# Kernel optimization log

Measured on AMD Instinct MI355X. Metric: run time of the kernel, lower is better.

Reference implementation:

```python
import jax, jax.numpy as jnp
import numpy as np

N_NODES = 50000
N_EDGES = 1600000
D_IN = 128
D_OUT = 128
K_HOPS = 2


def setup_inputs() -> dict:
    key = jax.random.key(0)
    k1, k2, k3, k4 = jax.random.split(key, 4)
    feat = jax.random.normal(k1, (N_NODES, D_IN), dtype=jnp.float32)
    src = jax.random.randint(k2, (N_EDGES,), 0, N_NODES, dtype=jnp.int64)
    dst = jax.random.randint(k3, (N_EDGES,), 0, N_NODES, dtype=jnp.int64)
    # Linear params (xavier_uniform for W, zeros for b, as in reset_parameters)
    limit = float(np.sqrt(6.0 / (D_IN + D_OUT)))
    W = jax.random.uniform(k4, (D_OUT, D_IN), minval=-limit, maxval=limit, dtype=jnp.float32)
    b = jnp.zeros((D_OUT,), dtype=jnp.float32)
    return {"feat": feat, "src": src, "dst": dst, "W": W, "b": b}


def reference(feat, src, dst, W, b):
    # in-degrees: number of edges pointing into each node, clamped at 1
    ones = jnp.ones((src.shape[0],), dtype=jnp.float32)
    degs = jax.ops.segment_sum(ones, dst, num_segments=N_NODES)
    norm = jnp.clip(degs, 1.0, None) ** -0.5  # [N]
    norm = norm[:, None]  # [N,1]
    for _ in range(K_HOPS):
        feat = feat * norm                      # D^{-1/2} scale
        msg = feat[src]                         # copy_u: [E, D]
        feat = jax.ops.segment_sum(msg, dst, num_segments=N_NODES)  # sum into dst
        feat = feat * norm                      # D^{-1/2} scale
    # fc: Linear(in_feats, out_feats)
    return feat @ W.T + b
```

## Files before the change

### kernel.cpp

```cpp
#include <hip/hip_runtime.h>
#include <hip/hip_bf16.h>

#define NN 50000
#define NE 1600000
#define DD 128
#define NB 196
#define NCH 256
#define PER 6250
#define NT 8
#define TS 6250

typedef short bfrag __attribute__((ext_vector_type(8)));
typedef float ffrag __attribute__((ext_vector_type(4)));
typedef float f32x2 __attribute__((ext_vector_type(2)));

__device__ __forceinline__ float bf2f(unsigned short u) {
    union { unsigned int i; float f; } c; c.i = ((unsigned int)u) << 16; return c.f;
}
__device__ __forceinline__ unsigned short f2bf(float f) {
    __hip_bfloat16 h = __float2bfloat16(f);
    union { __hip_bfloat16 h; unsigned short u; } c; c.h = h; return c.u;
}
__device__ __forceinline__ int insane_bf16(unsigned short u) {
    unsigned e = (u >> 7) & 0xFF;
    return (e == 0xFF) || (e >= 0x8E);
}

__global__ void k_detect(const int* __restrict__ srcw, const int* __restrict__ dstw,
                         const unsigned short* __restrict__ feat16,
                         const unsigned short* __restrict__ w16,
                         int* __restrict__ flags) {
    __shared__ int s_idx, s_feat, s_w;
    int tid = threadIdx.x;
    if (tid == 0) { s_idx = 0; s_feat = 0; s_w = 0; }
    __syncthreads();
    if (tid < 64) {
        int v = srcw[2 * tid + 1] | dstw[2 * tid + 1];
        if (v) atomicOr(&s_idx, 1);
    }
    if (insane_bf16(feat16[2 * tid]) || insane_bf16(feat16[2 * tid + 512]))
        atomicOr(&s_feat, 1);
    if (insane_bf16(w16[2 * tid]) || insane_bf16(w16[2 * tid + 512]))
        atomicOr(&s_w, 1);
    __syncthreads();
    if (tid == 0) { flags[0] = (s_idx == 0) ? 1 : 0; flags[1] = s_feat; flags[2] = s_w; }
}

__device__ __forceinline__ int load_idx(const void* p, int e, int is64) {
    long long v = is64 ? ((const long long*)p)[e] : (long long)((const int*)p)[e];
    int i = (int)v;
    return (i < 0) ? 0 : (i >= NN ? NN - 1 : i);
}

__global__ __launch_bounds__(256) void k_count(const void* __restrict__ dst,
        int* __restrict__ cnt, const int* __restrict__ flags) {
    __shared__ int lc[NB];
    int c = blockIdx.x, tid = threadIdx.x;
    if (tid < NB) lc[tid] = 0;
    __syncthreads();
    int lo = c * PER, hi = lo + PER; if (hi > NE) hi = NE;
    int is64 = flags[0];
    for (int e = lo + tid; e < hi; e += 256)
        atomicAdd(&lc[load_idx(dst, e, is64) >> 8], 1);
    __syncthreads();
    if (tid < NB) cnt[tid * NCH + c] = lc[tid];
}

__global__ __launch_bounds__(256) void k_scan2(const int* __restrict__ cnt,
        int* __restrict__ loff, int* __restrict__ binsum) {
    __shared__ int buf[256];
    int b = blockIdx.x, tid = threadIdx.x;
    int v = cnt[b * NCH + tid];
    buf[tid] = v;
    __syncthreads();
    for (int off = 1; off < 256; off <<= 1) {
        int t = (tid >= off) ? buf[tid - off] : 0;
        __syncthreads();
        buf[tid] += t;
        __syncthreads();
    }
    loff[b * NCH + tid] = buf[tid] - v;
    if (tid == 255) binsum[b] = buf[255];
}

__global__ __launch_bounds__(256) void k_scanbin(const int* __restrict__ binsum,
        int* __restrict__ binoff, int* __restrict__ rowptr) {
    __shared__ int buf[256];
    int tid = threadIdx.x;
    int v = (tid < NB) ? binsum[tid] : 0;
    buf[tid] = v;
    __syncthreads();
    for (int off = 1; off < 256; off <<= 1) {
        int t = (tid >= off) ? buf[tid - off] : 0;
        __syncthreads();
        buf[tid] += t;
        __syncthreads();
    }
    if (tid < NB) binoff[tid] = buf[tid] - v;
    if (tid == NB - 1) binoff[NB] = buf[tid];
    if (tid == 0) rowptr[NN] = NE;
}

__global__ __launch_bounds__(256) void k_stage(const void* __restrict__ src,
        const void* __restrict__ dst, const int* __restrict__ binoff,
        const int* __restrict__ loff, unsigned* __restrict__ staged,
        const int* __restrict__ flags) {
    __shared__ int cur[NB];
    int c = blockIdx.x, tid = threadIdx.x;
    if (tid < NB) cur[tid] = binoff[tid] + loff[tid * NCH + c];
    __syncthreads();
    int lo = c * PER, hi = lo + PER; if (hi > NE) hi = NE;
    int is64 = flags[0];
    for (int e = lo + tid; e < hi; e += 256) {
        int d = load_idx(dst, e, is64);
        int s = load_idx(src, e, is64);
        int pos = atomicAdd(&cur[d >> 8], 1);
        staged[pos] = ((unsigned)(d & 255) << 16) | (unsigned)s;
    }
}

__global__ __launch_bounds__(512) void k_fill(const unsigned* __restrict__ staged,
        const int* __restrict__ binoff, int* __restrict__ rowptr,
        float* __restrict__ norm, int* __restrict__ srclist) {
    __shared__ int cnt4[256 * NT];
    __shared__ int ntot[256];
    int b = blockIdx.x, tid = threadIdx.x;
    int lo = binoff[b], hi = binoff[b + 1];
    for (int i = tid; i < 256 * NT; i += 512) cnt4[i] = 0;
    __syncthreads();
    for (int k = lo + tid; k < hi; k += 512) {
        unsigned u = staged[k];
        atomicAdd(&cnt4[(u >> 16) * NT + (int)(u & 0xffff) / TS], 1);
    }
    __syncthreads();
    if (tid < 256) {
        int s = 0;
        #pragma unroll
        for (int t = 0; t < NT; ++t) s += cnt4[tid * NT + t];
        ntot[tid] = s;
    }
    __syncthreads();
    for (int off = 1; off < 256; off <<= 1) {
        int t = 0;
        if (tid < 256 && tid >= off) t = ntot[tid - off];
        __syncthreads();
        if (tid < 256) ntot[tid] += t;
        __syncthreads();
    }
    if (tid < 256) {
        int deg = 0;
        #pragma unroll
        for (int t = 0; t < NT; ++t) deg += cnt4[tid * NT + t];
        int start = lo + ntot[tid] - deg;
        int n = b * 256 + tid;
        if (n < NN) {
            rowptr[n] = start;
            norm[n] = rsqrtf(fmaxf((float)deg, 1.0f));
        }
        int c = start;
        #pragma unroll
        for (int t = 0; t < NT; ++t) {
            int v = cnt4[tid * NT + t];
            cnt4[tid * NT + t] = c;
            c += v;
        }
    }
    __syncthreads();
    for (int k = lo + tid; k < hi; k += 512) {
        unsigned u = staged[k];
        int s = (int)(u & 0xffff);
        int pos = atomicAdd(&cnt4[(u >> 16) * NT + s / TS], 1);
        srclist[pos] = s << 7;
    }
}

__global__ void k_prescale(const void* __restrict__ feat,
                           const float* __restrict__ norm,
                           unsigned short* __restrict__ X,
                           const int* __restrict__ flags) {
    int i = blockIdx.x * 256 + threadIdx.x;
    if (i >= NN * DD / 4) return;
    float nm = norm[i >> 5];
    float4 v;
    if (flags[1]) {
        v = ((const float4*)feat)[i];
    } else {
        ushort4 f = ((const ushort4*)feat)[i];
        v.x = bf2f(f.x); v.y = bf2f(f.y); v.z = bf2f(f.z); v.w = bf2f(f.w);
    }
    ushort4 o;
    o.x = f2bf(v.x * nm); o.y = f2bf(v.y * nm);
    o.z = f2bf(v.z * nm); o.w = f2bf(v.w * nm);
    ((ushort4*)X)[i] = o;
}

__device__ __forceinline__ f32x2 bfpair(unsigned u) {
    union { unsigned i; float f; } lo, hi;
    lo.i = u << 16;
    hi.i = u & 0xffff0000u;
    f32x2 r; r[0] = lo.f; r[1] = hi.f; return r;
}
__device__ __forceinline__ void accp(f32x2* a, uint4 v) {
    a[0] += bfpair(v.x);
    a[1] += bfpair(v.y);
    a[2] += bfpair(v.z);
    a[3] += bfpair(v.w);
}

__global__ __launch_bounds__(256, 6) void k_gather(const unsigned short* __restrict__ Xin,
        const int* __restrict__ rowptr, const int* __restrict__ srclist,
        const float* __restrict__ norm, unsigned short* __restrict__ outp,
        int mode) {
    int wid = (blockIdx.x * 256 + threadIdx.x) >> 6;
    int lane = threadIdx.x & 63;
    if (wid >= NN) return;
    int beg = rowptr[wid], end = rowptr[wid + 1];
    int g = lane >> 4;
    int c8 = (lane & 15) << 3;
    const unsigned short* xb = Xin + c8;
    f32x2 a[4];
    #pragma unroll
    for (int k = 0; k < 4; ++k) a[k] = (f32x2){0.f, 0.f};

    int j = beg + g;
    for (; j + 28 < end; j += 32) {
        int s0 = srclist[j];
        int s1 = srclist[j + 4];
        int s2 = srclist[j + 8];
        int s3 = srclist[j + 12];
        int s4 = srclist[j + 16];
        int s5 = srclist[j + 20];
        int s6 = srclist[j + 24];
        int s7 = srclist[j + 28];
        uint4 r0 = *(const uint4*)(xb + s0);
        uint4 r1 = *(const uint4*)(xb + s1);
        uint4 r2 = *(const uint4*)(xb + s2);
        uint4 r3 = *(const uint4*)(xb + s3);
        uint4 r4 = *(const uint4*)(xb + s4);
        uint4 r5 = *(const uint4*)(xb + s5);
        uint4 r6 = *(const uint4*)(xb + s6);
        uint4 r7 = *(const uint4*)(xb + s7);
        accp(a, r0); accp(a, r1); accp(a, r2); accp(a, r3);
        accp(a, r4); accp(a, r5); accp(a, r6); accp(a, r7);
    }
    for (; j + 12 < end; j += 16) {
        int s0 = srclist[j];
        int s1 = srclist[j + 4];
        int s2 = srclist[j + 8];
        int s3 = srclist[j + 12];
        uint4 r0 = *(const uint4*)(xb + s0);
        uint4 r1 = *(const uint4*)(xb + s1);
        uint4 r2 = *(const uint4*)(xb + s2);
        uint4 r3 = *(const uint4*)(xb + s3);
        accp(a, r0); accp(a, r1); accp(a, r2); accp(a, r3);
    }
    for (; j < end; j += 4) {
        int s = srclist[j];
        uint4 v = *(const uint4*)(xb + s);
        accp(a, v);
    }
    #pragma unroll
    for (int k = 0; k < 4; ++k) {
        a[k][0] += __shfl_xor(a[k][0], 16);
        a[k][1] += __shfl_xor(a[k][1], 16);
        a[k][0] += __shfl_xor(a[k][0], 32);
        a[k][1] += __shfl_xor(a[k][1], 32);
    }

    if (g == 0) {
        float nm = norm[wid];
        float sc = (mode == 0) ? nm * nm : nm;
        uint4 o;
        o.x = ((unsigned)f2bf(a[0][1] * sc) << 16) | (unsigned)f2bf(a[0][0] * sc);
        o.y = ((unsigned)f2bf(a[1][1] * sc) << 16) | (unsigned)f2bf(a[1][0] * sc);
        o.z = ((unsigned)f2bf(a[2][1] * sc) << 16) | (unsigned)f2bf(a[2][0] * sc);
        o.w = ((unsigned)f2bf(a[3][1] * sc) << 16) | (unsigned)f2bf(a[3][0] * sc);
        *(uint4*)(outp + wid * DD + c8) = o;
    }
}

__global__ __launch_bounds__(256) void k_gemm2(const unsigned short* __restrict__ Yb,
        const void* __restrict__ Wp, const void* __restrict__ bp,
        void* __restrict__ outp, const int* __restrict__ flags) {
    __shared__ unsigned short Wl[DD * 136];
    int tid = threadIdx.x;
    int wf32 = flags[2], of32 = flags[1];

    for (int i = tid; i < 8192; i += 256) {
        int r = i >> 6, cc = i & 63;
        unsigned pk;
        if (wf32) {
            float2 w = ((const float2*)Wp)[i];
            pk = ((unsigned)f2bf(w.y) << 16) | (unsigned)f2bf(w.x);
        } else {
            pk = ((const unsigned*)Wp)[i];
        }
        *(unsigned*)&Wl[r * 136 + cc * 2] = pk;
    }
    __syncthreads();

    int wave = tid >> 6, lane = tid & 63;
    int nb = blockIdx.x * 64 + wave * 16;
    int m = lane & 15, quad = lane >> 4;
    int arow = nb + m; if (arow >= NN) arow = NN - 1;
    const unsigned short* arp = Yb + arow * DD + quad * 8;

    ffrag acc[8];
    #pragma unroll
    for (int t = 0; t < 8; ++t) acc[t] = (ffrag){0.f, 0.f, 0.f, 0.f};

    #pragma unroll
    for (int c = 0; c < 4; ++c) {
        bfrag af = *(const bfrag*)(arp + c * 32);
        #pragma unroll
        for (int t = 0; t < 8; ++t) {
            bfrag bf = *(const bfrag*)&Wl[(t * 16 + m) * 136 + c * 32 + quad * 8];
            acc[t] = __builtin_amdgcn_mfma_f32_16x16x32_bf16(af, bf, acc[t], 0, 0, 0);
        }
    }

    #pragma unroll
    for (int t = 0; t < 8; ++t) {
        int o = t * 16 + m;
        float bias = wf32 ? ((const float*)bp)[o] : bf2f(((const unsigned short*)bp)[o]);
        #pragma unroll
        for (int r = 0; r < 4; ++r) {
            int n = nb + quad * 4 + r;
            if (n < NN) {
                float v = acc[t][r] + bias;
                if (of32) ((float*)outp)[n * DD + o] = v;
                else      ((unsigned short*)outp)[n * DD + o] = f2bf(v);
            }
        }
    }
}

extern "C" void kernel_launch(void* const* d_in, const int* in_sizes, int n_in,
                              void* d_out, int out_size, void* d_ws, size_t ws_size,
                              hipStream_t stream) {
    const void* feat = d_in[0];
    const void* src  = d_in[1];
    const void* dst  = d_in[2];
    const void* W    = d_in[3];
    const void* b    = d_in[4];

    char* wsb = (char*)d_ws;
    int*   flags   = (int*)wsb;
    int*   rowptr  = (int*)(wsb + 64);
    float* norm    = (float*)(wsb + 200128);
    int*   cnt     = (int*)(wsb + 400128);
    int*   loff    = (int*)(wsb + 600832);
    int*   binsum  = (int*)(wsb + 801536);
    int*   binoff  = (int*)(wsb + 802560);
    int*   srclist = (int*)(wsb + 803584);
    unsigned short* X1 = (unsigned short*)(wsb + 7203584);
    unsigned short* X2 = (unsigned short*)(wsb + 20003584);
    unsigned* staged   = (unsigned*)(wsb + 20003584);

    k_detect<<<1, 256, 0, stream>>>((const int*)src, (const int*)dst,
                                    (const unsigned short*)feat,
                                    (const unsigned short*)W, flags);
    k_count<<<NCH, 256, 0, stream>>>(dst, cnt, flags);
    k_scan2<<<NB, 256, 0, stream>>>(cnt, loff, binsum);
    k_scanbin<<<1, 256, 0, stream>>>(binsum, binoff, rowptr);
    k_stage<<<NCH, 256, 0, stream>>>(src, dst, binoff, loff, staged, flags);
    k_fill<<<NB, 512, 0, stream>>>(staged, binoff, rowptr, norm, srclist);
    k_prescale<<<(NN * DD / 4 + 255) / 256, 256, 0, stream>>>(feat, norm, X1, flags);
    k_gather<<<(NN + 3) / 4, 256, 0, stream>>>(X1, rowptr, srclist, norm, X2, 0);
    k_gather<<<(NN + 3) / 4, 256, 0, stream>>>(X2, rowptr, srclist, norm, X1, 1);
    k_gemm2<<<(NN + 63) / 64, 256, 0, stream>>>(X1, W, b, d_out, flags);
}
```

Before: 274.2 us.

## Load edge indices cooperatively per wave and shuffle them, padding with a zero row

The gather kernel now has each lane load one source index per batch of up to 64 edges and hands them out with wave shuffles. Each group then issues eight feature loads at once, and out-of-range slots point at a zero-filled pad row, so the three tail loops with dependent index loads go away. The prescale kernel writes zero pad rows after both feature buffers, the X2 and staged offsets move to make room, and the fill kernel's source binning goes from 8 to 4 tiles. The launch-bounds occupancy hint is also dropped. In exchange, nodes with few edges waste loads on the zero row, and register pressure may change.

```diff
diff --git a/kernel.cpp b/kernel.cpp
--- a/kernel.cpp
+++ b/kernel.cpp
@@ -7,8 +7,9 @@
 #define NB 196
 #define NCH 256
 #define PER 6250
-#define NT 8
-#define TS 6250
+#define NT 4
+#define TS 12500
+#define ZOFF (NN * DD)
 
 typedef short bfrag __attribute__((ext_vector_type(8)));
 typedef float ffrag __attribute__((ext_vector_type(4)));
@@ -177,9 +178,17 @@
 __global__ void k_prescale(const void* __restrict__ feat,
                            const float* __restrict__ norm,
                            unsigned short* __restrict__ X,
+                           unsigned short* __restrict__ X2,
                            const int* __restrict__ flags) {
     int i = blockIdx.x * 256 + threadIdx.x;
-    if (i >= NN * DD / 4) return;
+    const int total = NN * DD / 4;
+    if (i >= total) {
+        int r = i - total;
+        ushort4 z; z.x = 0; z.y = 0; z.z = 0; z.w = 0;
+        if (r < 32)      ((ushort4*)X)[total + r] = z;
+        else if (r < 64) ((ushort4*)X2)[total + (r - 32)] = z;
+        return;
+    }
     float nm = norm[i >> 5];
     float4 v;
     if (flags[1]) {
@@ -207,7 +216,7 @@
     a[3] += bfpair(v.w);
 }
 
-__global__ __launch_bounds__(256, 6) void k_gather(const unsigned short* __restrict__ Xin,
+__global__ __launch_bounds__(256) void k_gather(const unsigned short* __restrict__ Xin,
         const int* __restrict__ rowptr, const int* __restrict__ srclist,
         const float* __restrict__ norm, unsigned short* __restrict__ outp,
         int mode) {
@@ -222,42 +231,37 @@
     #pragma unroll
     for (int k = 0; k < 4; ++k) a[k] = (f32x2){0.f, 0.f};
 
-    int j = beg + g;
-    for (; j + 28 < end; j += 32) {
-        int s0 = srclist[j];
-        int s1 = srclist[j + 4];
-        int s2 = srclist[j + 8];
-        int s3 = srclist[j + 12];
-        int s4 = srclist[j + 16];
-        int s5 = srclist[j + 20];
-        int s6 = srclist[j + 24];
-        int s7 = srclist[j + 28];
-        uint4 r0 = *(const uint4*)(xb + s0);
-        uint4 r1 = *(const uint4*)(xb + s1);
-        uint4 r2 = *(const uint4*)(xb + s2);
-        uint4 r3 = *(const uint4*)(xb + s3);
-        uint4 r4 = *(const uint4*)(xb + s4);
-        uint4 r5 = *(const uint4*)(xb + s5);
-        uint4 r6 = *(const uint4*)(xb + s6);
-        uint4 r7 = *(const uint4*)(xb + s7);
-        accp(a, r0); accp(a, r1); accp(a, r2); accp(a, r3);
-        accp(a, r4); accp(a, r5); accp(a, r6); accp(a, r7);
-    }
-    for (; j + 12 < end; j += 16) {
-        int s0 = srclist[j];
-        int s1 = srclist[j + 4];
-        int s2 = srclist[j + 8];
-        int s3 = srclist[j + 12];
-        uint4 r0 = *(const uint4*)(xb + s0);
-        uint4 r1 = *(const uint4*)(xb + s1);
-        uint4 r2 = *(const uint4*)(xb + s2);
-        uint4 r3 = *(const uint4*)(xb + s3);
-        accp(a, r0); accp(a, r1); accp(a, r2); accp(a, r3);
-    }
-    for (; j < end; j += 4) {
-        int s = srclist[j];
-        uint4 v = *(const uint4*)(xb + s);
-        accp(a, v);
+    int j = beg;
+    while (j < end) {
+        int n = end - j;
+        if (n > 64) n = 64;
+        int li = (lane < n) ? lane : (n - 1);
+        int sv = srclist[j + li];
+        {
+            uint4 r[8];
+            #pragma unroll
+            for (int i = 0; i < 8; ++i) {
+                int k = g + 4 * i;
+                int s = __shfl(sv, k);
+                s = (k < n) ? s : ZOFF;
+                r[i] = *(const uint4*)(xb + s);
+            }
+            #pragma unroll
+            for (int i = 0; i < 8; ++i) accp(a, r[i]);
+        }
+        if (n > 32) {
+            uint4 r[8];
+            #pragma unroll
+            for (int i = 0; i < 8; ++i) {
+                int k = 32 + g + 4 * i;
+                int s = __shfl(sv, k);
+                s = (k < n) ? s : ZOFF;
+                r[i] = *(const uint4*)(xb + s);
+            }
+            #pragma unroll
+            for (int i = 0; i < 8; ++i) accp(a, r[i]);
+        }
+        j += n;
     }
     #pragma unroll
     for (int k = 0; k < 4; ++k) {
@@ -354,8 +358,8 @@
     int*   binoff  = (int*)(wsb + 802560);
     int*   srclist = (int*)(wsb + 803584);
     unsigned short* X1 = (unsigned short*)(wsb + 7203584);
-    unsigned short* X2 = (unsigned short*)(wsb + 20003584);
-    unsigned* staged   = (unsigned*)(wsb + 20003584);
+    unsigned short* X2 = (unsigned short*)(wsb + 20003840);
+    unsigned* staged   = (unsigned*)(wsb + 20003840);
 
     k_detect<<<1, 256, 0, stream>>>((const int*)src, (const int*)dst,
                                     (const unsigned short*)feat,
@@ -365,7 +369,7 @@
     k_scanbin<<<1, 256, 0, stream>>>(binsum, binoff, rowptr);
     k_stage<<<NCH, 256, 0, stream>>>(src, dst, binoff, loff, staged, flags);
     k_fill<<<NB, 512, 0, stream>>>(staged, binoff, rowptr, norm, srclist);
-    k_prescale<<<(NN * DD / 4 + 255) / 256, 256, 0, stream>>>(feat, norm, X1, flags);
+    k_prescale<<<NN * DD / 4 / 256 + 1, 256, 0, stream>>>(feat, norm, X1, X2, flags);
     k_gather<<<(NN + 3) / 4, 256, 0, stream>>>(X1, rowptr, srclist, norm, X2, 0);
     k_gather<<<(NN + 3) / 4, 256, 0, stream>>>(X2, rowptr, srclist, norm, X1, 1);
     k_gemm2<<<(NN + 63) / 64, 256, 0, stream>>>(X1, W, b, d_out, flags);
```

New measurement: 259.5 us. 5.4% less time.

## Gather two nodes per 16-lane group, interleaved across source-range tiles

Applied to the files above, without the earlier changes.

The gather kernel now gives each 16-lane group two whole destination nodes instead of splitting one node's edges across four groups. It walks both nodes' edges tile by tile, using per-node source-range boundaries (4 tiles of 12500 source rows) that the fill kernel now records, so all wavefronts touch a similar region of X at the same time. This drops the cross-group shuffle reduction and is meant to improve L2 locality. In exchange it adds per-lane load imbalance from varying degrees, a shorter unroll, an extra int4 table per node, and it removes the occupancy hint from the launch bounds.

```diff
diff --git a/kernel.cpp b/kernel.cpp
--- a/kernel.cpp
+++ b/kernel.cpp
@@ -7,8 +7,10 @@
 #define NB 196
 #define NCH 256
 #define PER 6250
-#define NT 8
-#define TS 6250
+#define NT 4
+#define TS 12500
+#define GWAVE 6252
+#define GBLK 1563
 
 typedef short bfrag __attribute__((ext_vector_type(8)));
 typedef float ffrag __attribute__((ext_vector_type(4)));
@@ -121,6 +123,7 @@
 
 __global__ __launch_bounds__(512) void k_fill(const unsigned* __restrict__ staged,
         const int* __restrict__ binoff, int* __restrict__ rowptr,
+        int4* __restrict__ tptr,
         float* __restrict__ norm, int* __restrict__ srclist) {
     __shared__ int cnt4[256 * NT];
     __shared__ int ntot[256];
@@ -133,12 +136,9 @@
         atomicAdd(&cnt4[(u >> 16) * NT + (int)(u & 0xffff) / TS], 1);
     }
     __syncthreads();
-    if (tid < 256) {
-        int s = 0;
-        #pragma unroll
-        for (int t = 0; t < NT; ++t) s += cnt4[tid * NT + t];
-        ntot[tid] = s;
-    }
+    if (tid < 256)
+        ntot[tid] = cnt4[tid * NT] + cnt4[tid * NT + 1]
+                  + cnt4[tid * NT + 2] + cnt4[tid * NT + 3];
     __syncthreads();
     for (int off = 1; off < 256; off <<= 1) {
         int t = 0;
@@ -148,22 +148,25 @@
         __syncthreads();
     }
     if (tid < 256) {
-        int deg = 0;
-        #pragma unroll
-        for (int t = 0; t < NT; ++t) deg += cnt4[tid * NT + t];
+        int v0 = cnt4[tid * NT], v1 = cnt4[tid * NT + 1];
+        int v2 = cnt4[tid * NT + 2], v3 = cnt4[tid * NT + 3];
+        int deg = v0 + v1 + v2 + v3;
         int start = lo + ntot[tid] - deg;
         int n = b * 256 + tid;
+        int4 tp;
+        tp.x = start;
+        tp.y = start + v0;
+        tp.z = start + v0 + v1;
+        tp.w = start + v0 + v1 + v2;
         if (n < NN) {
             rowptr[n] = start;
             norm[n] = rsqrtf(fmaxf((float)deg, 1.0f));
-        }
-        int c = start;
-        #pragma unroll
-        for (int t = 0; t < NT; ++t) {
-            int v = cnt4[tid * NT + t];
-            cnt4[tid * NT + t] = c;
-            c += v;
-        }
+            tptr[n] = tp;
+        }
+        cnt4[tid * NT + 0] = tp.x;
+        cnt4[tid * NT + 1] = tp.y;
+        cnt4[tid * NT + 2] = tp.z;
+        cnt4[tid * NT + 3] = tp.w;
     }
     __syncthreads();
     for (int k = lo + tid; k < hi; k += 512) {
@@ -207,75 +210,90 @@
     a[3] += bfpair(v.w);
 }
 
-__global__ __launch_bounds__(256, 6) void k_gather(const unsigned short* __restrict__ Xin,
-        const int* __restrict__ rowptr, const int* __restrict__ srclist,
+__global__ __launch_bounds__(256) void k_gather(const unsigned short* __restrict__ Xin,
+        const int* __restrict__ rowptr, const int4* __restrict__ tptr,
+        const int* __restrict__ srclist,
         const float* __restrict__ norm, unsigned short* __restrict__ outp,
         int mode) {
     int wid = (blockIdx.x * 256 + threadIdx.x) >> 6;
     int lane = threadIdx.x & 63;
-    if (wid >= NN) return;
-    int beg = rowptr[wid], end = rowptr[wid + 1];
-    int g = lane >> 4;
+    int grp = lane >> 4;
     int c8 = (lane & 15) << 3;
     const unsigned short* xb = Xin + c8;
-    f32x2 a[4];
-    #pragma unroll
-    for (int k = 0; k < 4; ++k) a[k] = (f32x2){0.f, 0.f};
-
-    int j = beg + g;
-    for (; j + 28 < end; j += 32) {
-        int s0 = srclist[j];
-        int s1 = srclist[j + 4];
-        int s2 = srclist[j + 8];
-        int s3 = srclist[j + 12];
-        int s4 = srclist[j + 16];
-        int s5 = srclist[j + 20];
-        int s6 = srclist[j + 24];
-        int s7 = srclist[j + 28];
-        uint4 r0 = *(const uint4*)(xb + s0);
-        uint4 r1 = *(const uint4*)(xb + s1);
-        uint4 r2 = *(const uint4*)(xb + s2);
-        uint4 r3 = *(const uint4*)(xb + s3);
-        uint4 r4 = *(const uint4*)(xb + s4);
-        uint4 r5 = *(const uint4*)(xb + s5);
-        uint4 r6 = *(const uint4*)(xb + s6);
-        uint4 r7 = *(const uint4*)(xb + s7);
-        accp(a, r0); accp(a, r1); accp(a, r2); accp(a, r3);
-        accp(a, r4); accp(a, r5); accp(a, r6); accp(a, r7);
-    }
-    for (; j + 12 < end; j += 16) {
-        int s0 = srclist[j];
-        int s1 = srclist[j + 4];
-        int s2 = srclist[j + 8];
-        int s3 = srclist[j + 12];
-        uint4 r0 = *(const uint4*)(xb + s0);
-        uint4 r1 = *(const uint4*)(xb + s1);
-        uint4 r2 = *(const uint4*)(xb + s2);
-        uint4 r3 = *(const uint4*)(xb + s3);
-        accp(a, r0); accp(a, r1); accp(a, r2); accp(a, r3);
-    }
-    for (; j < end; j += 4) {
-        int s = srclist[j];
-        uint4 v = *(const uint4*)(xb + s);
-        accp(a, v);
-    }
-    #pragma unroll
-    for (int k = 0; k < 4; ++k) {
-        a[k][0] += __shfl_xor(a[k][0], 16);
-        a[k][1] += __shfl_xor(a[k][1], 16);
-        a[k][0] += __shfl_xor(a[k][0], 32);
-        a[k][1] += __shfl_xor(a[k][1], 32);
-    }
-
-    if (g == 0) {
-        float nm = norm[wid];
+
+    int n0 = wid * 8 + grp;
+    int n1 = n0 + 4;
+    bool val0 = (n0 < NN), val1 = (n1 < NN);
+
+    int4 tp0 = val0 ? tptr[n0] : (int4){0, 0, 0, 0};
+    int  e0  = val0 ? rowptr[n0 + 1] : 0;
+    int4 tp1 = val1 ? tptr[n1] : (int4){0, 0, 0, 0};
+    int  e1  = val1 ? rowptr[n1 + 1] : 0;
+
+    int st0[5] = {tp0.x, tp0.y, tp0.z, tp0.w, e0};
+    int st1[5] = {tp1.x, tp1.y, tp1.z, tp1.w, e1};
+
+    f32x2 a0[4], a1[4];
+    #pragma unroll
+    for (int k = 0; k < 4; ++k) { a0[k] = (f32x2){0.f, 0.f}; a1[k] = (f32x2){0.f, 0.f}; }
+
+    #pragma unroll
+    for (int t = 0; t < 4; ++t) {
+        int j = st0[t], je = st0[t + 1];
+        for (; j + 3 < je; j += 4) {
+            int s0 = srclist[j];
+            int s1 = srclist[j + 1];
+            int s2 = srclist[j + 2];
+            int s3 = srclist[j + 3];
+            uint4 r0 = *(const uint4*)(xb + s0);
+            uint4 r1 = *(const uint4*)(xb + s1);
+            uint4 r2 = *(const uint4*)(xb + s2);
+            uint4 r3 = *(const uint4*)(xb + s3);
+            accp(a0, r0); accp(a0, r1); accp(a0, r2); accp(a0, r3);
+        }
+        for (; j < je; ++j) {
+            int s = srclist[j];
+            uint4 v = *(const uint4*)(xb + s);
+            accp(a0, v);
+        }
+        j = st1[t]; je = st1[t + 1];
+        for (; j + 3 < je; j += 4) {
+            int s0 = srclist[j];
+            int s1 = srclist[j + 1];
+            int s2 = srclist[j + 2];
+            int s3 = srclist[j + 3];
+            uint4 r0 = *(const uint4*)(xb + s0);
+            uint4 r1 = *(const uint4*)(xb + s1);
+            uint4 r2 = *(const uint4*)(xb + s2);
+            uint4 r3 = *(const uint4*)(xb + s3);
+            accp(a1, r0); accp(a1, r1); accp(a1, r2); accp(a1, r3);
+        }
+        for (; j < je; ++j) {
+            int s = srclist[j];
+            uint4 v = *(const uint4*)(xb + s);
+            accp(a1, v);
+        }
+    }
+
+    if (val0) {
+        float nm = norm[n0];
         float sc = (mode == 0) ? nm * nm : nm;
         uint4 o;
-        o.x = ((unsigned)f2bf(a[0][1] * sc) << 16) | (unsigned)f2bf(a[0][0] * sc);
-        o.y = ((unsigned)f2bf(a[1][1] * sc) << 16) | (unsigned)f2bf(a[1][0] * sc);
-        o.z = ((unsigned)f2bf(a[2][1] * sc) << 16) | (unsigned)f2bf(a[2][0] * sc);
-        o.w = ((unsigned)f2bf(a[3][1] * sc) << 16) | (unsigned)f2bf(a[3][0] * sc);
-        *(uint4*)(outp + wid * DD + c8) = o;
+        o.x = ((unsigned)f2bf(a0[0][1] * sc) << 16) | (unsigned)f2bf(a0[0][0] * sc);
+        o.y = ((unsigned)f2bf(a0[1][1] * sc) << 16) | (unsigned)f2bf(a0[1][0] * sc);
+        o.z = ((unsigned)f2bf(a0[2][1] * sc) << 16) | (unsigned)f2bf(a0[2][0] * sc);
+        o.w = ((unsigned)f2bf(a0[3][1] * sc) << 16) | (unsigned)f2bf(a0[3][0] * sc);
+        *(uint4*)(outp + n0 * DD + c8) = o;
+    }
+    if (val1) {
+        float nm = norm[n1];
+        float sc = (mode == 0) ? nm * nm : nm;
+        uint4 o;
+        o.x = ((unsigned)f2bf(a1[0][1] * sc) << 16) | (unsigned)f2bf(a1[0][0] * sc);
+        o.y = ((unsigned)f2bf(a1[1][1] * sc) << 16) | (unsigned)f2bf(a1[1][0] * sc);
+        o.z = ((unsigned)f2bf(a1[2][1] * sc) << 16) | (unsigned)f2bf(a1[2][0] * sc);
+        o.w = ((unsigned)f2bf(a1[3][1] * sc) << 16) | (unsigned)f2bf(a1[3][0] * sc);
+        *(uint4*)(outp + n1 * DD + c8) = o;
     }
 }
 
@@ -352,10 +370,11 @@
     int*   loff    = (int*)(wsb + 600832);
     int*   binsum  = (int*)(wsb + 801536);
     int*   binoff  = (int*)(wsb + 802560);
-    int*   srclist = (int*)(wsb + 803584);
-    unsigned short* X1 = (unsigned short*)(wsb + 7203584);
-    unsigned short* X2 = (unsigned short*)(wsb + 20003584);
-    unsigned* staged   = (unsigned*)(wsb + 20003584);
+    int4*  tptr    = (int4*)(wsb + 803584);
+    int*   srclist = (int*)(wsb + 1603584);
+    unsigned short* X1 = (unsigned short*)(wsb + 8003584);
+    unsigned short* X2 = (unsigned short*)(wsb + 20803840);
+    unsigned* staged   = (unsigned*)(wsb + 20803840);
 
     k_detect<<<1, 256, 0, stream>>>((const int*)src, (const int*)dst,
                                     (const unsigned short*)feat,
@@ -364,9 +383,9 @@
     k_scan2<<<NB, 256, 0, stream>>>(cnt, loff, binsum);
     k_scanbin<<<1, 256, 0, stream>>>(binsum, binoff, rowptr);
     k_stage<<<NCH, 256, 0, stream>>>(src, dst, binoff, loff, staged, flags);
-    k_fill<<<NB, 512, 0, stream>>>(staged, binoff, rowptr, norm, srclist);
+    k_fill<<<NB, 512, 0, stream>>>(staged, binoff, rowptr, tptr, norm, srclist);
     k_prescale<<<(NN * DD / 4 + 255) / 256, 256, 0, stream>>>(feat, norm, X1, flags);
-    k_gather<<<(NN + 3) / 4, 256, 0, stream>>>(X1, rowptr, srclist, norm, X2, 0);
-    k_gather<<<(NN + 3) / 4, 256, 0, stream>>>(X2, rowptr, srclist, norm, X1, 1);
+    k_gather<<<GBLK, 256, 0, stream>>>(X1, rowptr, tptr, srclist, norm, X2, 0);
+    k_gather<<<GBLK, 256, 0, stream>>>(X2, rowptr, tptr, srclist, norm, X1, 1);
     k_gemm2<<<(NN + 63) / 64, 256, 0, stream>>>(X1, W, b, d_out, flags);
 }
```

Result: faster. 235.6 us (-14.1%).
